# Kernel optimization log

Measured on AMD Instinct MI355X. Metric: run time of the kernel, lower is better.

Reference implementation:

```python
import jax, jax.numpy as jnp
import numpy as np


def _split(x):
    # x: (bs, c, 16, 16) -> 16 patches of (bs, c, 4, 4), ordered patch[4*r + col]
    bs, c, H, W = x.shape
    t = x.reshape(bs, c, 4, 4, 4, 4)          # (bs, c, Rblk, h, Cblk, w)
    t = jnp.transpose(t, (2, 4, 0, 1, 3, 5))  # (Rblk, Cblk, bs, c, h, w)
    return t.reshape(16, bs, c, 4, 4)


def _cat(p):
    # p: (16, bs, c, 4, 4). Faithful to original cat_tensor: group 0 (rows 0:4)
    # is concatenated but DROPPED; output is (bs, c, 12, 16).
    n, bs, c, h, w = p.shape
    rows = p.reshape(4, 4, bs, c, h, w)                                  # (group, j, ...)
    rows = jnp.transpose(rows, (0, 2, 3, 4, 1, 5)).reshape(4, bs, c, h, 4 * w)
    return jnp.concatenate([rows[1], rows[2], rows[3]], axis=2)          # (bs, c, 12, 16)


def setup_inputs() -> dict:
    key = jax.random.key(0)
    ks = jax.random.split(key, 4)
    bs, c, d = 128, 512, 32  # d = max(L=32, channel // reduction = 32)
    x = jax.random.normal(ks[0], (bs, c, 16, 16), jnp.float32)
    x1 = jax.random.normal(ks[1], (bs, c, 16, 16), jnp.float32)
    fc_w = jax.random.normal(ks[2], (d, c), jnp.float32) / np.float32(np.sqrt(c))
    fc_b = jnp.zeros((d,), jnp.float32)
    fcs_w = jax.random.normal(ks[3], (2, c, d), jnp.float32) / np.float32(np.sqrt(d))
    fcs_b = jnp.zeros((2, c), jnp.float32)
    return {"x": x, "x1": x1, "fc_w": fc_w, "fc_b": fc_b,
            "fcs_w": fcs_w, "fcs_b": fcs_b}


def reference(x, x1, fc_w, fc_b, fcs_w, fcs_b):
    out_rgb = _split(x)        # (16, bs, c, 4, 4)
    out_freq = _split(x1)      # (16, bs, c, 4, 4)
    patchU = _split(x + x1)    # U = sum(conv_outs) = x + x1

    S = patchU.mean((-1, -2))                                    # (16, bs, c)
    Z = jnp.einsum('pbc,dc->pbd', S, fc_w) + fc_b                # (16, bs, d)
    logits = jnp.einsum('pbd,kcd->kpbc', Z, fcs_w) + fcs_b[:, None, None, :]  # (2,16,bs,c)
    attn = jax.nn.softmax(logits, axis=0)                        # softmax over branch dim

    feats = jnp.stack([out_rgb, out_freq], 0)                    # (2, 16, bs, c, 4, 4)
    V = attn[..., None, None] * feats                            # (2, 16, bs, c, 4, 4)

    # Faithful to source: v1 = V_rgb[i] + patch_rgb[i][i] (batch-i slice of patch i)
    idx = jnp.arange(16)
    extra_rgb = out_rgb[idx, idx][:, None]    # (16, 1, c, 4, 4)
    extra_freq = out_freq[idx, idx][:, None]  # (16, 1, c, 4, 4)
    v1 = V[0] + extra_rgb                     # (16, bs, c, 4, 4)
    v2 = V[1] + extra_freq

    return _cat(v1), _cat(v2)                 # each (bs, c, 12, 16)
```

## Files before the change

### kernel.cpp

```cpp
#include <hip/hip_runtime.h>


#define BS 128
#define C  512
#define D  32

typedef float f32x4 __attribute__((ext_vector_type(4)));

__global__ __launch_bounds__(256) void skatt_diag(
    const float* __restrict__ x, const float* __restrict__ x1,
    float* __restrict__ E)
{
    const int src = blockIdx.y;
    const float* in = src ? x1 : x;
    float* Eo = E + (size_t)src * (C * 192);

    const int flat = blockIdx.x * 256 + threadIdx.x;
    const int ch  = flat / 48;
    const int rem = flat - ch * 48;
    const int g   = (rem >> 4) + 1;
    const int h   = (rem >> 2) & 3;
    const int j   = rem & 3;

    const size_t src_ofs = (size_t)(4 * g + j) * (C * 256) + ch * 256 + (4 * g + h) * 16 + 4 * j;
    float4 v = *(const float4*)(in + src_ofs);
    *(float4*)(Eo + ch * 192 + rem * 4) = v;
}

__global__ __launch_bounds__(256) void skatt_meanz(
    const float* __restrict__ x, const float* __restrict__ x1,
    const float* __restrict__ fc_w,
    float* __restrict__ P)
{
    const int g = blockIdx.x + 1;
    const int b = blockIdx.y;
    const int q = blockIdx.z;
    const int t = threadIdx.x;

    __shared__ float s_s[128][4];
    __shared__ float s_w[128][33];

    {
        const int j  = t & 3;
        const int cl = t >> 2;
        const size_t base = (size_t)b * (C * 256);
        #pragma unroll
        for (int i = 0; i < 2; ++i) {
            const int ch = q * 128 + cl + i * 64;
            const float* px = x  + base + ch * 256 + (4 * g) * 16 + j * 4;
            const float* p1 = x1 + base + ch * 256 + (4 * g) * 16 + j * 4;
            float s = 0.f;
            #pragma unroll
            for (int h = 0; h < 4; ++h) {
                float4 a  = *(const float4*)(px + h * 16);
                float4 c2 = *(const float4*)(p1 + h * 16);
                s += (a.x + c2.x) + (a.y + c2.y) + (a.z + c2.z) + (a.w + c2.w);
            }
            s_s[cl + i * 64][j] = s * (1.0f / 16.0f);
        }
    }

    {
        const int d  = t >> 3;
        const int c4 = t & 7;
        const float* wsrc = fc_w + d * C + q * 128 + c4 * 16;
        #pragma unroll
        for (int k = 0; k < 4; ++k) {
            float4 v = *(const float4*)(wsrc + k * 4);
            const int c = c4 * 16 + k * 4;
            s_w[c + 0][d] = v.x;
            s_w[c + 1][d] = v.y;
            s_w[c + 2][d] = v.z;
            s_w[c + 3][d] = v.w;
        }
    }
    __syncthreads();

    if (t < 128) {
        const int j = t >> 5, d = t & 31;
        float a0 = 0.f, a1 = 0.f, a2 = 0.f, a3 = 0.f;
        #pragma unroll 8
        for (int c = 0; c < 128; c += 4) {
            a0 += s_s[c + 0][j] * s_w[c + 0][d];
            a1 += s_s[c + 1][j] * s_w[c + 1][d];
            a2 += s_s[c + 2][j] * s_w[c + 2][d];
            a3 += s_s[c + 3][j] * s_w[c + 3][d];
        }
        P[((size_t)((g - 1) * BS + b) * 4 + j) * 128 + q * 32 + d] =
            (a0 + a1) + (a2 + a3);
    }
}

__global__ __launch_bounds__(256) void skatt_outf(
    const float* __restrict__ x, const float* __restrict__ x1,
    const float* __restrict__ E, const float* __restrict__ P,
    const float* __restrict__ fc_b,
    const float* __restrict__ fcs_w, const float* __restrict__ fcs_b,
    float* __restrict__ out)
{
    const int q = blockIdx.x;
    const int b = blockIdx.y;
    const int t = threadIdx.x;
    const int ch0 = q * 32;

    __shared__ float s_z[3][128];
    __shared__ float s_wt[32][33];
    __shared__ float s_bd[32];
    __shared__ float s_A[32][12];

    if (t < 96) {
        const int g1 = t >> 5, j = (t >> 3) & 3, d4 = t & 7;
        const f32x4* P4 = (const f32x4*)P;
        const size_t base4 = (size_t)(g1 * BS + b) * 128;
        f32x4 acc = ((const f32x4*)fc_b)[d4];
        #pragma unroll
        for (int qq = 0; qq < 4; ++qq) {
            f32x4 pv = P4[base4 + j * 32 + qq * 8 + d4];
            acc.x += pv.x; acc.y += pv.y; acc.z += pv.z; acc.w += pv.w;
        }
        *(f32x4*)(&s_z[g1][j * 32 + d4 * 4]) = acc;
    }
    {
        const f32x4* w04 = (const f32x4*)(fcs_w + (size_t)ch0 * D);
        const f32x4* w14 = (const f32x4*)(fcs_w + (size_t)C * D + (size_t)ch0 * D);
        f32x4 a  = w04[t];
        f32x4 bb = w14[t];
        const int ch = t >> 3, d0 = (t & 7) * 4;
        s_wt[d0 + 0][ch] = a.x - bb.x;
        s_wt[d0 + 1][ch] = a.y - bb.y;
        s_wt[d0 + 2][ch] = a.z - bb.z;
        s_wt[d0 + 3][ch] = a.w - bb.w;
    }
    if (t < 32) s_bd[t] = fcs_b[ch0 + t] - fcs_b[C + ch0 + t];
    __syncthreads();

    {
        const int ch_l = t & 31, k = t >> 5;
        float wd[D];
        #pragma unroll
        for (int d = 0; d < D; ++d) wd[d] = s_wt[d][ch_l];
        const float bdv = s_bd[ch_l];

        {
            const int g1 = k >> 2, j = k & 3;
            float acc = bdv;
            #pragma unroll
            for (int d = 0; d < D; ++d) acc += s_z[g1][j * 32 + d] * wd[d];
            s_A[ch_l][k] = 1.0f / (1.0f + __expf(-acc));
        }
        if (k < 4) {
            const int p = k + 8;
            const int g1 = p >> 2, j = p & 3;
            float acc = bdv;
            #pragma unroll
            for (int d = 0; d < D; ++d) acc += s_z[g1][j * 32 + d] * wd[d];
            s_A[ch_l][p] = 1.0f / (1.0f + __expf(-acc));
        }
    }
    __syncthreads();

    const size_t xbase = (size_t)b * (C * 256);
    const size_t obase = (size_t)b * (C * 192);
    const size_t out2_off = (size_t)BS * C * 192;
    const float* E1 = E;
    const float* E2 = E + (size_t)C * 192;

    #pragma unroll
    for (int i = 0; i < 6; ++i) {
        const int v    = t + i * 256;
        const int ch_l = v / 48;
        const int rem  = v - ch_l * 48;
        const int ch   = ch0 + ch_l;
        const int j    = rem & 3;
        const int g1   = rem >> 4;

        const float at0 = s_A[ch_l][g1 * 4 + j];
        const float at1 = 1.0f - at0;

        const size_t xofs = xbase + ch * 256 + 64 + rem * 4;
        float4 a  = *(const float4*)(x  + xofs);
        float4 c2 = *(const float4*)(x1 + xofs);
        const size_t eofs = (size_t)ch * 192 + rem * 4;
        float4 e1 = *(const float4*)(E1 + eofs);
        float4 e2 = *(const float4*)(E2 + eofs);

        float4 r1, r2;
        r1.x = at0 * a.x + e1.x;   r2.x = at1 * c2.x + e2.x;
        r1.y = at0 * a.y + e1.y;   r2.y = at1 * c2.y + e2.y;
        r1.z = at0 * a.z + e1.z;   r2.z = at1 * c2.z + e2.z;
        r1.w = at0 * a.w + e1.w;   r2.w = at1 * c2.w + e2.w;

        const size_t oofs = obase + ch * 192 + rem * 4;
        *(float4*)(out + oofs) = r1;
        *(float4*)(out + out2_off + oofs) = r2;
    }
}

extern "C" void kernel_launch(void* const* d_in, const int* in_sizes, int n_in,
                              void* d_out, int out_size, void* d_ws, size_t ws_size,
                              hipStream_t stream) {
    const float* x     = (const float*)d_in[0];
    const float* x1    = (const float*)d_in[1];
    const float* fc_w  = (const float*)d_in[2];
    const float* fc_b  = (const float*)d_in[3];
    const float* fcs_w = (const float*)d_in[4];
    const float* fcs_b = (const float*)d_in[5];
    float* out = (float*)d_out;

    float* P = (float*)d_ws;
    float* E = P + 196608;

    skatt_diag <<<dim3(96, 2),    256, 0, stream>>>(x, x1, E);
    skatt_meanz<<<dim3(3, BS, 4), 256, 0, stream>>>(x, x1, fc_w, P);
    skatt_outf <<<dim3(16, BS),   256, 0, stream>>>(x, x1, E, P, fc_b, fcs_w, fcs_b, out);
}
```

Baseline: 58.36 us.

## Split mean reduction from fc matmul and merge fc with diag-gather kernel

The first kernel now only computes the patch means and writes them to a workspace. A new middle kernel does the full 512-wide fc projection per (group, batch), adds the bias, and in extra blocks copies the diagonal extra patches. This removes the partial-sum reduction in the final kernel. It also stops reloading fc_w slices across four channel-quarter blocks, though each middle block now loads all of fc_w into about 75KB of shared memory, which limits occupancy. The final output stores become nontemporal.

```diff
diff --git a/kernel.cpp b/kernel.cpp
--- a/kernel.cpp
+++ b/kernel.cpp
@@ -7,94 +7,109 @@
 
 typedef float f32x4 __attribute__((ext_vector_type(4)));
 
-__global__ __launch_bounds__(256) void skatt_diag(
+__global__ __launch_bounds__(256) void skatt_means(
     const float* __restrict__ x, const float* __restrict__ x1,
-    float* __restrict__ E)
-{
-    const int src = blockIdx.y;
-    const float* in = src ? x1 : x;
-    float* Eo = E + (size_t)src * (C * 192);
-
-    const int flat = blockIdx.x * 256 + threadIdx.x;
-    const int ch  = flat / 48;
-    const int rem = flat - ch * 48;
-    const int g   = (rem >> 4) + 1;
-    const int h   = (rem >> 2) & 3;
-    const int j   = rem & 3;
-
-    const size_t src_ofs = (size_t)(4 * g + j) * (C * 256) + ch * 256 + (4 * g + h) * 16 + 4 * j;
-    float4 v = *(const float4*)(in + src_ofs);
-    *(float4*)(Eo + ch * 192 + rem * 4) = v;
-}
-
-__global__ __launch_bounds__(256) void skatt_meanz(
-    const float* __restrict__ x, const float* __restrict__ x1,
-    const float* __restrict__ fc_w,
-    float* __restrict__ P)
+    float* __restrict__ S)
 {
     const int g = blockIdx.x + 1;
     const int b = blockIdx.y;
     const int q = blockIdx.z;
     const int t = threadIdx.x;
-
-    __shared__ float s_s[128][4];
-    __shared__ float s_w[128][33];
-
-    {
-        const int j  = t & 3;
-        const int cl = t >> 2;
-        const size_t base = (size_t)b * (C * 256);
+    const int j  = t & 3;
+    const int cl = t >> 2;
+
+    const size_t base = (size_t)b * (C * 256);
+    float* Sgb = S + ((size_t)(g - 1) * BS + b) * (4 * C);
+
+    #pragma unroll
+    for (int i = 0; i < 2; ++i) {
+        const int ch = q * 128 + cl + i * 64;
+        const float* px = x  + base + ch * 256 + (4 * g) * 16 + j * 4;
+        const float* p1 = x1 + base + ch * 256 + (4 * g) * 16 + j * 4;
+        float s = 0.f;
         #pragma unroll
-        for (int i = 0; i < 2; ++i) {
-            const int ch = q * 128 + cl + i * 64;
-            const float* px = x  + base + ch * 256 + (4 * g) * 16 + j * 4;
-            const float* p1 = x1 + base + ch * 256 + (4 * g) * 16 + j * 4;
-            float s = 0.f;
+        for (int h = 0; h < 4; ++h) {
+            float4 a  = *(const float4*)(px + h * 16);
+            float4 c2 = *(const float4*)(p1 + h * 16);
+            s += (a.x + c2.x) + (a.y + c2.y) + (a.z + c2.z) + (a.w + c2.w);
+        }
+        Sgb[j * C + ch] = s * (1.0f / 16.0f);
+    }
+}
+
+__global__ __launch_bounds__(256) void skatt_mid(
+    const float* __restrict__ x, const float* __restrict__ x1,
+    const float* __restrict__ S, const float* __restrict__ fc_w,
+    const float* __restrict__ fc_b,
+    float* __restrict__ E, float* __restrict__ Z)
+{
+    __shared__ float s_w[C][33];
+    __shared__ float s_S[4 * C];
+
+    const int blk = blockIdx.x;
+    const int t = threadIdx.x;
+
+    if (blk < 384) {
+        const int g1 = blk >> 7, b = blk & 127;
+
+        {
+            const int d  = t >> 3;
+            const int c0 = (t & 7) * 64;
+            const float4* wr = (const float4*)(fc_w + d * C + c0);
             #pragma unroll
-            for (int h = 0; h < 4; ++h) {
-                float4 a  = *(const float4*)(px + h * 16);
-                float4 c2 = *(const float4*)(p1 + h * 16);
-                s += (a.x + c2.x) + (a.y + c2.y) + (a.z + c2.z) + (a.w + c2.w);
+            for (int k = 0; k < 16; ++k) {
+                float4 v = wr[k];
+                const int c = c0 + k * 4;
+                s_w[c + 0][d] = v.x;
+                s_w[c + 1][d] = v.y;
+                s_w[c + 2][d] = v.z;
+                s_w[c + 3][d] = v.w;
             }
-            s_s[cl + i * 64][j] = s * (1.0f / 16.0f);
-        }
-    }
-
-    {
-        const int d  = t >> 3;
-        const int c4 = t & 7;
-        const float* wsrc = fc_w + d * C + q * 128 + c4 * 16;
-        #pragma unroll
-        for (int k = 0; k < 4; ++k) {
-            float4 v = *(const float4*)(wsrc + k * 4);
-            const int c = c4 * 16 + k * 4;
-            s_w[c + 0][d] = v.x;
-            s_w[c + 1][d] = v.y;
-            s_w[c + 2][d] = v.z;
-            s_w[c + 3][d] = v.w;
-        }
-    }
-    __syncthreads();
-
-    if (t < 128) {
-        const int j = t >> 5, d = t & 31;
-        float a0 = 0.f, a1 = 0.f, a2 = 0.f, a3 = 0.f;
-        #pragma unroll 8
-        for (int c = 0; c < 128; c += 4) {
-            a0 += s_s[c + 0][j] * s_w[c + 0][d];
-            a1 += s_s[c + 1][j] * s_w[c + 1][d];
-            a2 += s_s[c + 2][j] * s_w[c + 2][d];
-            a3 += s_s[c + 3][j] * s_w[c + 3][d];
-        }
-        P[((size_t)((g - 1) * BS + b) * 4 + j) * 128 + q * 32 + d] =
-            (a0 + a1) + (a2 + a3);
+        }
+        {
+            const float4* Ss = (const float4*)(S + ((size_t)g1 * BS + b) * (4 * C));
+            ((float4*)s_S)[t]       = Ss[t];
+            ((float4*)s_S)[t + 256] = Ss[t + 256];
+        }
+        __syncthreads();
+
+        if (t < 128) {
+            const int j = t >> 5, d = t & 31;
+            const float* sr = s_S + j * C;
+            float a0 = 0.f, a1 = 0.f, a2 = 0.f, a3 = 0.f;
+            #pragma unroll 8
+            for (int c = 0; c < C; c += 4) {
+                a0 += sr[c + 0] * s_w[c + 0][d];
+                a1 += sr[c + 1] * s_w[c + 1][d];
+                a2 += sr[c + 2] * s_w[c + 2][d];
+                a3 += sr[c + 3] * s_w[c + 3][d];
+            }
+            Z[((size_t)(g1 * BS + b) * 4 + j) * 32 + d] =
+                (a0 + a1) + (a2 + a3) + fc_b[d];
+        }
+    } else {
+        const int blk2 = blk - 384;
+        const int src  = blk2 >= 96;
+        const int bb   = src ? blk2 - 96 : blk2;
+        const float* in = src ? x1 : x;
+        float* Eo = E + (size_t)src * (C * 192);
+
+        const int flat = bb * 256 + t;
+        const int ch  = flat / 48;
+        const int rem = flat - ch * 48;
+        const int g   = (rem >> 4) + 1;
+        const int h   = (rem >> 2) & 3;
+        const int j   = rem & 3;
+
+        const size_t src_ofs = (size_t)(4 * g + j) * (C * 256) + ch * 256 + (4 * g + h) * 16 + 4 * j;
+        float4 v = *(const float4*)(in + src_ofs);
+        *(float4*)(Eo + ch * 192 + rem * 4) = v;
     }
 }
 
 __global__ __launch_bounds__(256) void skatt_outf(
     const float* __restrict__ x, const float* __restrict__ x1,
-    const float* __restrict__ E, const float* __restrict__ P,
-    const float* __restrict__ fc_b,
+    const float* __restrict__ E, const float* __restrict__ Z,
     const float* __restrict__ fcs_w, const float* __restrict__ fcs_b,
     float* __restrict__ out)
 {
@@ -110,15 +125,8 @@
 
     if (t < 96) {
         const int g1 = t >> 5, j = (t >> 3) & 3, d4 = t & 7;
-        const f32x4* P4 = (const f32x4*)P;
-        const size_t base4 = (size_t)(g1 * BS + b) * 128;
-        f32x4 acc = ((const f32x4*)fc_b)[d4];
-        #pragma unroll
-        for (int qq = 0; qq < 4; ++qq) {
-            f32x4 pv = P4[base4 + j * 32 + qq * 8 + d4];
-            acc.x += pv.x; acc.y += pv.y; acc.z += pv.z; acc.w += pv.w;
-        }
-        *(f32x4*)(&s_z[g1][j * 32 + d4 * 4]) = acc;
+        f32x4 v = ((const f32x4*)Z)[(size_t)(g1 * BS + b) * 32 + j * 8 + d4];
+        *(f32x4*)(&s_z[g1][j * 32 + d4 * 4]) = v;
     }
     {
         const f32x4* w04 = (const f32x4*)(fcs_w + (size_t)ch0 * D);
@@ -184,15 +192,15 @@
         float4 e1 = *(const float4*)(E1 + eofs);
         float4 e2 = *(const float4*)(E2 + eofs);
 
-        float4 r1, r2;
+        f32x4 r1, r2;
         r1.x = at0 * a.x + e1.x;   r2.x = at1 * c2.x + e2.x;
         r1.y = at0 * a.y + e1.y;   r2.y = at1 * c2.y + e2.y;
         r1.z = at0 * a.z + e1.z;   r2.z = at1 * c2.z + e2.z;
         r1.w = at0 * a.w + e1.w;   r2.w = at1 * c2.w + e2.w;
 
         const size_t oofs = obase + ch * 192 + rem * 4;
-        *(float4*)(out + oofs) = r1;
-        *(float4*)(out + out2_off + oofs) = r2;
+        __builtin_nontemporal_store(r1, (f32x4*)(out + oofs));
+        __builtin_nontemporal_store(r2, (f32x4*)(out + out2_off + oofs));
     }
 }
 
@@ -207,10 +215,11 @@
     const float* fcs_b = (const float*)d_in[5];
     float* out = (float*)d_out;
 
-    float* P = (float*)d_ws;
-    float* E = P + 196608;
-
-    skatt_diag <<<dim3(96, 2),    256, 0, stream>>>(x, x1, E);
-    skatt_meanz<<<dim3(3, BS, 4), 256, 0, stream>>>(x, x1, fc_w, P);
-    skatt_outf <<<dim3(16, BS),   256, 0, stream>>>(x, x1, E, P, fc_b, fcs_w, fcs_b, out);
-}
+    float* S = (float*)d_ws;
+    float* E = S + 786432;
+    float* Z = E + 196608;
+
+    skatt_means<<<dim3(3, BS, 4), 256, 0, stream>>>(x, x1, S);
+    skatt_mid  <<<576,            256, 0, stream>>>(x, x1, S, fc_w, fc_b, E, Z);
+    skatt_outf <<<dim3(16, BS),   256, 0, stream>>>(x, x1, E, Z, fcs_w, fcs_b, out);
+}
```

Result: slower. 63.61 us (+9.0%).
